# Performance work log

Measured on AMD Instinct MI355X. Metric: run time of the kernel, lower is better.

## Reference

```python
import jax, jax.numpy as jnp
import numpy as np

B, N, D = 2, 16384, 512
H = 256          # gated-attention hidden dim
C, K = 4, 8      # num classes, descriptions per class
EPS = 1e-12


def _l2norm(x):
    return x / jnp.clip(jnp.linalg.norm(x, axis=-1, keepdims=True), EPS)


def setup_inputs() -> dict:
    key = jax.random.key(0)
    ks = jax.random.split(key, 12)
    inp = {
        'x_s': jax.random.normal(ks[0], (B, N, D), jnp.float32),
        'coord_s': jax.random.uniform(ks[1], (B, N, 2), jnp.float32),
        'x_l': jax.random.normal(ks[2], (B, N, D), jnp.float32),
        'coord_l': jax.random.uniform(ks[3], (B, N, 2), jnp.float32),
        # visual_proj: Linear(D, D), stored as [in, out] (apply x @ W + b)
        'W_proj': jax.random.normal(ks[4], (D, D), jnp.float32) / np.sqrt(D),
        'b_proj': jnp.zeros((D,), jnp.float32),
        # frozen, L2-normalized text description features [C, K, D]
        'desc_feats': _l2norm(jax.random.normal(ks[5], (C, K, D), jnp.float32)),
        # GatedAttentionPooling params ([in, out] layout)
        'Wv': jax.random.normal(ks[6], (D, H), jnp.float32) / np.sqrt(D),
        'bv': jnp.zeros((H,), jnp.float32),
        'Wu': jax.random.normal(ks[7], (D, H), jnp.float32) / np.sqrt(D),
        'bu': jnp.zeros((H,), jnp.float32),
        'w_attn': jax.random.normal(ks[8], (H,), jnp.float32) / np.sqrt(H),
        'b_attn': jnp.zeros((), jnp.float32),
    }
    return inp


def _class_scores(xp, desc_feats):
    # xp: [B,N,D] normalized projected patches; desc_feats: [C,K,D]
    scale = desc_feats.shape[-1] ** (-0.5)
    sim = jnp.einsum('bnd,ckd->bnck', xp, desc_feats) * scale  # [B,N,C,K]
    attn = jax.nn.softmax(sim, axis=-1)
    # scores_c = <xp, attn @ desc_c> collapsed without materializing [B,N,C,D]
    return jnp.einsum('bnck,ckd,bnd->bnc', attn, desc_feats, xp)  # [B,N,C]


def _gated_pool(feats, Wv, bv, Wu, bu, w_attn, b_attn):
    # feats: [B,N,D]
    A_V = jnp.tanh(feats @ Wv + bv)                 # [B,N,H]
    A_U = jax.nn.sigmoid(feats @ Wu + bu)           # [B,N,H]
    A = (A_V * A_U) @ w_attn + b_attn               # [B,N]
    A = jax.nn.softmax(A, axis=1)
    return jnp.einsum('bn,bnd->bd', A, feats)       # [B,D]


def reference(x_s, coord_s, x_l, coord_l, W_proj, b_proj, desc_feats,
              Wv, bv, Wu, bu, w_attn, b_attn):
    # coords are unused by the compute path (kept for signature fidelity)
    x_s_proj = _l2norm(_l2norm(x_s) @ W_proj + b_proj)
    x_l_proj = _l2norm(_l2norm(x_l) @ W_proj + b_proj)

    class_scores_s = _class_scores(x_s_proj, desc_feats)  # [B,N,C]
    class_scores_l = _class_scores(x_l_proj, desc_feats)

    slide_s = _l2norm(_gated_pool(x_s_proj, Wv, bv, Wu, bu, w_attn, b_attn))
    slide_l = _l2norm(_gated_pool(x_l_proj, Wv, bv, Wu, bu, w_attn, b_attn))

    # text_features_low: per-class max over descriptions, L2-normalized
    text_feats = _l2norm(jnp.max(desc_feats, axis=1))      # [C,D]

    logits = slide_s @ text_feats.T + slide_l @ text_feats.T  # [B,C]
    Y_prob = jax.nn.softmax(logits, axis=1)
    Y_hat = jnp.argmax(Y_prob, axis=1)
    return Y_prob, Y_hat, class_scores_s, class_scores_l
```

## Files before the change

### kernel.cpp

```cpp
#include <hip/hip_runtime.h>
#include <math.h>

#define B_ 2
#define N_ 16384
#define D_ 512
#define C_ 4
#define K_ 8
#define ROWS (B_*N_)
#define ROWS2 (2*ROWS)
#define EPS_ 1e-12f

typedef unsigned short u16;
typedef unsigned int u32;
using short8  = __attribute__((ext_vector_type(8))) short;
using float4v = __attribute__((ext_vector_type(4))) float;

__device__ __forceinline__ u16 f2bf(float f) {
    union { float f; u32 u; } v; v.f = f;
    u32 r = v.u + 0x7fffu + ((v.u >> 16) & 1u);
    return (u16)(r >> 16);
}
__device__ __forceinline__ u32 pack2(float a, float b) {
    return (u32)f2bf(a) | ((u32)f2bf(b) << 16);
}
__device__ __forceinline__ float bf2f(u16 h) {
    union { u32 u; float f; } v; v.u = ((u32)h) << 16;
    return v.f;
}
__device__ __forceinline__ void load_lds16(const u16* g, u16* l) {
    __builtin_amdgcn_global_load_lds(
        (const __attribute__((address_space(1))) u32*)g,
        (__attribute__((address_space(3))) u32*)l, 16, 0, 0);
}
__device__ __forceinline__ void stage_rows8(const u16* gtile, u16* ldsTile, int g, int lane) {
    int rg = lane >> 3;
    int c  = (lane & 7) ^ rg;
    load_lds16(gtile + (size_t)(g * 8 + rg) * 512 + c * 8, ldsTile + g * 512);
}
#define AFRAG(lds, R, c) (*(const short8*)&(lds)[(R) * 64 + (((c) ^ ((R) & 7)) * 8)])

__global__ __launch_bounds__(256) void prep_weights_kernel(
    const float* __restrict__ Wp, const float* __restrict__ Wv, const float* __restrict__ Wu,
    const float* __restrict__ bv, const float* __restrict__ bu, const float* __restrict__ desc,
    u16* __restrict__ WpT, u16* __restrict__ WvuT, float* __restrict__ bvu,
    u16* __restrict__ descF)
{
    int idx = blockIdx.x * 256 + threadIdx.x;
    int n = idx >> 9, k = idx & 511;
    WpT[idx] = f2bf(Wp[k * 512 + n]);
    int tile = n >> 4, pair = tile >> 1, half = tile & 1, h = pair * 16 + (n & 15);
    WvuT[idx] = f2bf(half ? Wu[k * 256 + h] : Wv[k * 256 + h]);
    if (idx < 512) {
        int tl = idx >> 4, pr = tl >> 1, hf = tl & 1, hh = pr * 16 + (idx & 15);
        bvu[idx] = hf ? bu[hh] : bv[hh];
    }
    if (idx < 16384) {
        int j = idx & 7, l = (idx >> 3) & 63, g = (idx >> 9) & 1, kt = idx >> 10;
        descF[idx] = f2bf(desc[(size_t)(g * 16 + (l & 15)) * 512 + kt * 32 + (l >> 4) * 8 + j]);
    }
}

__global__ __launch_bounds__(256) void rownorm_cast_kernel(
    const float* __restrict__ x_s, const float* __restrict__ x_l, u16* __restrict__ xn)
{
    int wave = threadIdx.x >> 6, lane = threadIdx.x & 63;
    size_t row = (size_t)blockIdx.x * 4 + wave;
    const float* xr = (row < (size_t)ROWS) ? (x_s + row * D_)
                                           : (x_l + (row - ROWS) * D_);
    float4 a = *(const float4*)&xr[lane * 8];
    float4 b = *(const float4*)&xr[lane * 8 + 4];
    float s = a.x*a.x + a.y*a.y + a.z*a.z + a.w*a.w
            + b.x*b.x + b.y*b.y + b.z*b.z + b.w*b.w;
#pragma unroll
    for (int off = 32; off; off >>= 1) s += __shfl_xor(s, off, 64);
    float inv = 1.0f / fmaxf(sqrtf(s), EPS_);
    uint4 o;
    o.x = pack2(a.x * inv, a.y * inv);
    o.y = pack2(a.z * inv, a.w * inv);
    o.z = pack2(b.x * inv, b.y * inv);
    o.w = pack2(b.z * inv, b.w * inv);
    *(uint4*)&xn[row * D_ + lane * 8] = o;
}

__global__ __launch_bounds__(512, 2) void gemm_bias_kernel(
    const u16* __restrict__ A, const u16* __restrict__ Bt,
    const float* __restrict__ bias, u16* __restrict__ C)
{
    __shared__ u16 ldsA[128 * 64];
    __shared__ u16 ldsB[512 * 64];
    int t = threadIdx.x, wave = t >> 6, lane = t & 63;
    int lr = lane & 15, lq = lane >> 4;
    int wm = wave >> 2, wn = wave & 3;
    int M0 = blockIdx.x * 128;

    float4v acc[4][8];
#pragma unroll
    for (int i = 0; i < 4; ++i)
#pragma unroll
        for (int j = 0; j < 8; ++j)
#pragma unroll
            for (int r = 0; r < 4; ++r) acc[i][j][r] = 0.f;

    for (int k0 = 0; k0 < 512; k0 += 64) {
        const u16* Ab = A  + (size_t)M0 * 512 + k0;
        const u16* Bb = Bt + k0;
        stage_rows8(Ab, ldsA, wave * 2 + 0, lane);
        stage_rows8(Ab, ldsA, wave * 2 + 1, lane);
#pragma unroll
        for (int s = 0; s < 8; ++s) stage_rows8(Bb, ldsB, wave * 8 + s, lane);
        __syncthreads();
#pragma unroll
        for (int kt = 0; kt < 2; ++kt) {
            short8 af[4], bfr[8];
#pragma unroll
            for (int i = 0; i < 4; ++i)
                af[i] = AFRAG(ldsA, wm * 64 + i * 16 + lr, kt * 4 + lq);
#pragma unroll
            for (int j = 0; j < 8; ++j)
                bfr[j] = AFRAG(ldsB, wn * 128 + j * 16 + lr, kt * 4 + lq);
#pragma unroll
            for (int i = 0; i < 4; ++i)
#pragma unroll
                for (int j = 0; j < 8; ++j)
                    acc[i][j] = __builtin_amdgcn_mfma_f32_16x16x32_bf16(bfr[j], af[i], acc[i][j], 0, 0, 0);
        }
        __syncthreads();
    }

    int colbase = wn * 128;
    float4 b4[8];
#pragma unroll
    for (int j = 0; j < 8; ++j)
        b4[j] = *(const float4*)&bias[colbase + j * 16 + lq * 4];
#pragma unroll
    for (int i = 0; i < 4; ++i) {
        int m = M0 + wm * 64 + i * 16 + lr;
        u16* crow = C + (size_t)m * 512;
#pragma unroll
        for (int j = 0; j < 8; ++j) {
            int nb = colbase + j * 16 + lq * 4;
            uint2 o;
            o.x = pack2(acc[i][j][0] + b4[j].x, acc[i][j][1] + b4[j].y);
            o.y = pack2(acc[i][j][2] + b4[j].z, acc[i][j][3] + b4[j].w);
            *(uint2*)&crow[nb] = o;
        }
    }
}

__global__ __launch_bounds__(512, 2) void gatecls_kernel(
    const u16* __restrict__ A, const u16* __restrict__ Bt,
    const u16* __restrict__ descF,
    const float* __restrict__ bvu, const float* __restrict__ w_attn,
    float* __restrict__ invn, float* __restrict__ Araw,
    float* __restrict__ out10)
{
    __shared__ u16 ldsA[128 * 64];
    __shared__ u16 ldsB[512 * 64];
    int t = threadIdx.x, wave = t >> 6, lane = t & 63;
    int lr = lane & 15, lq = lane >> 4;
    int wm = wave >> 2, wn = wave & 3;
    int M0 = blockIdx.x * 128;

    float4v acc[4][8];
    float4v accS[2], accG;
#pragma unroll
    for (int i = 0; i < 4; ++i)
#pragma unroll
        for (int j = 0; j < 8; ++j)
#pragma unroll
            for (int r = 0; r < 4; ++r) acc[i][j][r] = 0.f;
#pragma unroll
    for (int r = 0; r < 4; ++r) { accS[0][r] = 0.f; accS[1][r] = 0.f; accG[r] = 0.f; }

    for (int k0 = 0; k0 < 512; k0 += 64) {
        const u16* Ab = A  + (size_t)M0 * 512 + k0;
        const u16* Bb = Bt + k0;
        stage_rows8(Ab, ldsA, wave * 2 + 0, lane);
        stage_rows8(Ab, ldsA, wave * 2 + 1, lane);
#pragma unroll
        for (int s = 0; s < 8; ++s) stage_rows8(Bb, ldsB, wave * 8 + s, lane);
        __syncthreads();
#pragma unroll
        for (int kt = 0; kt < 2; ++kt) {
            int ktg = (k0 >> 5) + kt;
            short8 d0 = *(const short8*)&descF[(ktg * 2 + 0) * 512 + lane * 8];
            short8 d1 = *(const short8*)&descF[(ktg * 2 + 1) * 512 + lane * 8];
            short8 afc = AFRAG(ldsA, wave * 16 + lr, kt * 4 + lq);
            accS[0] = __builtin_amdgcn_mfma_f32_16x16x32_bf16(afc, d0, accS[0], 0, 0, 0);
            accS[1] = __builtin_amdgcn_mfma_f32_16x16x32_bf16(afc, d1, accS[1], 0, 0, 0);
            accG    = __builtin_amdgcn_mfma_f32_16x16x32_bf16(afc, afc, accG, 0, 0, 0);
            short8 af[4], bfr[8];
#pragma unroll
            for (int i = 0; i < 4; ++i)
                af[i] = AFRAG(ldsA, wm * 64 + i * 16 + lr, kt * 4 + lq);
#pragma unroll
            for (int j = 0; j < 8; ++j)
                bfr[j] = AFRAG(ldsB, wn * 128 + j * 16 + lr, kt * 4 + lq);
#pragma unroll
            for (int i = 0; i < 4; ++i)
#pragma unroll
                for (int j = 0; j < 8; ++j)
                    acc[i][j] = __builtin_amdgcn_mfma_f32_16x16x32_bf16(bfr[j], af[i], acc[i][j], 0, 0, 0);
        }
        __syncthreads();
    }

    float* sInvF = (float*)ldsA;
    float* redA  = ((float*)ldsA) + 128;

#pragma unroll
    for (int r = 0; r < 4; ++r) {
        if (lr == lq * 4 + r) {
            float iv = 1.0f / fmaxf(sqrtf(accG[r]), EPS_);
            sInvF[wave * 16 + lq * 4 + r] = iv;
            invn[M0 + wave * 16 + lq * 4 + r] = iv;
        }
    }
    __syncthreads();

    {
        const float scale = 0.04419417382415922f;
        int side = (M0 >= ROWS) ? 1 : 0;
        float* cls = out10 + (size_t)side * ((size_t)ROWS * 4);
        int rbase = M0 - side * ROWS + wave * 16;
#pragma unroll
        for (int r = 0; r < 4; ++r) {
            int rloc = rbase + lq * 4 + r;
            float iv = sInvF[wave * 16 + lq * 4 + r];
            float sv0 = accS[0][r] * iv, sv1 = accS[1][r] * iv;
#pragma unroll
            for (int g = 0; g < 2; ++g) {
                float s = g ? sv1 : sv0;
                float ts = s * scale;
                float mx = ts;
                mx = fmaxf(mx, __shfl_xor(mx, 1, 64));
                mx = fmaxf(mx, __shfl_xor(mx, 2, 64));
                mx = fmaxf(mx, __shfl_xor(mx, 4, 64));
                float e = expf(ts - mx);
                float num = e * s, den = e;
                num += __shfl_xor(num, 1, 64); den += __shfl_xor(den, 1, 64);
                num += __shfl_xor(num, 2, 64); den += __shfl_xor(den, 2, 64);
                num += __shfl_xor(num, 4, 64); den += __shfl_xor(den, 4, 64);
                if ((lr & 7) == 0) {
                    int c = g * 2 + ((lr >> 3) & 1);
                    cls[(size_t)rloc * 4 + c] = num / den;
                }
            }
        }
    }

    int colbase = wn * 128;
    int hbase = colbase >> 1;
    float4 bv4[4], bu4[4], w4[4];
#pragma unroll
    for (int p = 0; p < 4; ++p) {
        int nv = colbase + p * 32 + lq * 4;
        bv4[p] = *(const float4*)&bvu[nv];
        bu4[p] = *(const float4*)&bvu[nv + 16];
        w4[p]  = *(const float4*)&w_attn[hbase + p * 16 + lq * 4];
    }
#pragma unroll
    for (int i = 0; i < 4; ++i) {
        int rloc = wm * 64 + i * 16 + lr;
        float iv = sInvF[rloc];
        float part = 0.f;
#pragma unroll
        for (int p = 0; p < 4; ++p) {
#pragma unroll
            for (int r = 0; r < 4; ++r) {
                float v = acc[i][2 * p][r] * iv + (&bv4[p].x)[r];
                float u = acc[i][2 * p + 1][r] * iv + (&bu4[p].x)[r];
                part += tanhf(v) * (&w4[p].x)[r] * (1.0f / (1.0f + expf(-u)));
            }
        }
        part += __shfl_xor(part, 16, 64);
        part += __shfl_xor(part, 32, 64);
        if (lq == 0) redA[wn * 128 + rloc] = part;
    }
    __syncthreads();
    if (t < 128) Araw[M0 + t] = redA[t] + redA[128 + t] + redA[256 + t] + redA[384 + t];
}

__global__ __launch_bounds__(256) void areduce_kernel(
    const float* __restrict__ Araw, float* __restrict__ part)
{
    __shared__ float red[256];
    int t = threadIdx.x, g = blockIdx.y;
    size_t i0 = (size_t)g * N_ + blockIdx.x * 512 + t * 2;
    float2 v = *(const float2*)&Araw[i0];
    red[t] = fmaxf(v.x, v.y); __syncthreads();
    for (int s = 128; s; s >>= 1) { if (t < s) red[t] = fmaxf(red[t], red[t + s]); __syncthreads(); }
    float m = red[0]; __syncthreads();
    red[t] = __expf(v.x - m) + __expf(v.y - m); __syncthreads();
    for (int s = 128; s; s >>= 1) { if (t < s) red[t] += red[t + s]; __syncthreads(); }
    if (t == 0) {
        int pi = g * 32 + blockIdx.x;
        part[pi * 2] = m;
        part[pi * 2 + 1] = red[0];
    }
}

__global__ __launch_bounds__(128) void acombine_kernel(
    const float* __restrict__ part, float* __restrict__ mg)
{
    int t = threadIdx.x;
    int g = t >> 5, j = t & 31;
    float m = part[(g * 32 + j) * 2];
    float s = part[(g * 32 + j) * 2 + 1];
    float mm = m;
#pragma unroll
    for (int off = 1; off < 32; off <<= 1) mm = fmaxf(mm, __shfl_xor(mm, off, 64));
    float sc = s * __expf(m - mm);
#pragma unroll
    for (int off = 1; off < 32; off <<= 1) sc += __shfl_xor(sc, off, 64);
    if (j == 0) {
        mg[g * 2] = mm;
        mg[g * 2 + 1] = 1.0f / sc;
    }
}

__global__ __launch_bounds__(256) void pool_kernel(
    const float* __restrict__ Araw, const float* __restrict__ invn,
    const float* __restrict__ mg, const u16* __restrict__ xpraw,
    float* __restrict__ slideAll)
{
    __shared__ float lds[4][512];
    int t = threadIdx.x, wave = t >> 6, lane = t & 63;
    int g = blockIdx.y;
    float m = mg[g * 2], is = mg[g * 2 + 1];
    size_t row0 = (size_t)g * N_ + (size_t)blockIdx.x * 256 + wave;
    float a[8] = {};
    for (int r = 0; r < 64; ++r) {
        size_t row = row0 + r * 4;
        float av = __expf(Araw[row] - m) * is * invn[row];
        uint4 pk = *(const uint4*)&xpraw[row * D_ + lane * 8];
        a[0] += av * bf2f((u16)pk.x); a[1] += av * bf2f((u16)(pk.x >> 16));
        a[2] += av * bf2f((u16)pk.y); a[3] += av * bf2f((u16)(pk.y >> 16));
        a[4] += av * bf2f((u16)pk.z); a[5] += av * bf2f((u16)(pk.z >> 16));
        a[6] += av * bf2f((u16)pk.w); a[7] += av * bf2f((u16)(pk.w >> 16));
    }
#pragma unroll
    for (int i = 0; i < 8; ++i) lds[wave][lane * 8 + i] = a[i];
    __syncthreads();
#pragma unroll
    for (int q = 0; q < 2; ++q) {
        int c = t * 2 + q;
        float s = lds[0][c] + lds[1][c] + lds[2][c] + lds[3][c];
        atomicAdd(&slideAll[(size_t)g * 512 + c], s);
    }
}

__global__ __launch_bounds__(512) void finalize_kernel(
    const float* __restrict__ slide_s, const float* __restrict__ slide_l,
    const float* __restrict__ desc, float* __restrict__ out)
{
    __shared__ float txt[4][512];
    __shared__ float ssn[2][512];
    __shared__ float sln[2][512];
    __shared__ float red[512];
    __shared__ float lg[8];
    int t = threadIdx.x;

    auto reduceSum = [&](float v) -> float {
        red[t] = v; __syncthreads();
        for (int s = 256; s; s >>= 1) { if (t < s) red[t] += red[t + s]; __syncthreads(); }
        float r = red[0]; __syncthreads();
        return r;
    };

    for (int c = 0; c < 4; ++c) {
        float m = -1e30f;
        for (int k = 0; k < 8; ++k) m = fmaxf(m, desc[((size_t)c * 8 + k) * 512 + t]);
        float ss = reduceSum(m * m);
        txt[c][t] = m / fmaxf(sqrtf(ss), EPS_);
    }
    for (int b = 0; b < 2; ++b) {
        float v = slide_s[b * 512 + t];
        float ss = reduceSum(v * v);
        ssn[b][t] = v / fmaxf(sqrtf(ss), EPS_);
        v = slide_l[b * 512 + t];
        ss = reduceSum(v * v);
        sln[b][t] = v / fmaxf(sqrtf(ss), EPS_);
    }
    __syncthreads();
    for (int b = 0; b < 2; ++b)
        for (int c = 0; c < 4; ++c) {
            float v = ssn[b][t] * txt[c][t] + sln[b][t] * txt[c][t];
            float s = reduceSum(v);
            if (t == 0) lg[b * 4 + c] = s;
        }
    __syncthreads();
    if (t < 2) {
        int b = t;
        float m = -1e30f;
        for (int c = 0; c < 4; ++c) m = fmaxf(m, lg[b * 4 + c]);
        float e[4]; float den = 0.f;
        for (int c = 0; c < 4; ++c) { e[c] = expf(lg[b * 4 + c] - m); den += e[c]; }
        int am = 0; float bm = -1.f;
        for (int c = 0; c < 4; ++c) {
            float pcl = e[c] / den;
            out[b * 4 + c] = pcl;
            if (pcl > bm) { bm = pcl; am = c; }
        }
        out[8 + b] = (float)am;
    }
}

extern "C" void kernel_launch(void* const* d_in, const int* in_sizes, int n_in,
                              void* d_out, int out_size, void* d_ws, size_t ws_size,
                              hipStream_t stream) {
    const float* x_s    = (const float*)d_in[0];
    const float* x_l    = (const float*)d_in[2];
    const float* W_proj = (const float*)d_in[4];
    const float* b_proj = (const float*)d_in[5];
    const float* desc   = (const float*)d_in[6];
    const float* Wv     = (const float*)d_in[7];
    const float* bv     = (const float*)d_in[8];
    const float* Wu     = (const float*)d_in[9];
    const float* bu     = (const float*)d_in[10];
    const float* w_attn = (const float*)d_in[11];
    float* out = (float*)d_out;

    char* w = (char*)d_ws;
    u16* xn        = (u16*)w;
    u16* xpraw     = (u16*)(w + 67108864);
    u16* WpT       = (u16*)(w + 134217728);
    u16* WvuT      = (u16*)(w + 134742016);
    u16* descF     = (u16*)(w + 135266304);
    float* bvu     = (float*)(w + 135299072);
    float* invn    = (float*)(w + 135301120);
    float* Araw    = (float*)(w + 135563264);
    float* part    = (float*)(w + 135825408);
    float* mg      = (float*)(w + 135826432);
    float* slideAll= (float*)(w + 135827456);

    hipMemsetAsync(slideAll, 0, 8192, stream);
    prep_weights_kernel<<<1024, 256, 0, stream>>>(W_proj, Wv, Wu, bv, bu, desc,
                                                  WpT, WvuT, bvu, descF);

    rownorm_cast_kernel<<<ROWS2 / 4, 256, 0, stream>>>(x_s, x_l, xn);
    gemm_bias_kernel<<<512, 512, 0, stream>>>(xn, WpT, b_proj, xpraw);
    gatecls_kernel<<<512, 512, 0, stream>>>(xpraw, WvuT, descF, bvu, w_attn,
                                            invn, Araw, out + 10);
    areduce_kernel<<<dim3(32, 4), 256, 0, stream>>>(Araw, part);
    acombine_kernel<<<1, 128, 0, stream>>>(part, mg);
    pool_kernel<<<dim3(64, 4), 256, 0, stream>>>(Araw, invn, mg, xpraw, slideAll);
    finalize_kernel<<<1, 512, 0, stream>>>(slideAll, slideAll + 1024, desc, out);
}
```

Before: 334.9 us.

## Split GEMMs into 128x128 N-tiles and move row norm into projection epilogue

Both GEMM kernels change from 128x512 tiles with 512 threads (512 blocks) to 128x128 tiles with 256 threads over a 4x512 grid. This raises block count and lowers the per-block LDS footprint, which should improve occupancy and load balance. The row sum-of-squares is now computed in the projection epilogue and accumulated with atomics, replacing the MFMA self-dot in gatecls; gate partials go to four per-N-tile buffers that areduce sums. The gate activations use fast __expf-based tanh and sigmoid. In exchange, A tiles are re-read four times per GEMM, and the change adds atomics and a larger memset.

```diff
diff --git a/kernel.cpp b/kernel.cpp
--- a/kernel.cpp
+++ b/kernel.cpp
@@ -27,6 +27,9 @@
     union { u32 u; float f; } v; v.u = ((u32)h) << 16;
     return v.f;
 }
+__device__ __forceinline__ float fsigmoid(float x) { return 1.0f / (1.0f + __expf(-x)); }
+__device__ __forceinline__ float ftanh(float x)    { return 1.0f - 2.0f / (__expf(2.0f * x) + 1.0f); }
+
 __device__ __forceinline__ void load_lds16(const u16* g, u16* l) {
     __builtin_amdgcn_global_load_lds(
         (const __attribute__((address_space(1))) u32*)g,
@@ -82,195 +85,200 @@
     *(uint4*)&xn[row * D_ + lane * 8] = o;
 }
 
-__global__ __launch_bounds__(512, 2) void gemm_bias_kernel(
+__global__ __launch_bounds__(256, 2) void gemm_bias_kernel(
     const u16* __restrict__ A, const u16* __restrict__ Bt,
-    const float* __restrict__ bias, u16* __restrict__ C)
+    const float* __restrict__ bias, u16* __restrict__ C, float* __restrict__ sumsq)
 {
     __shared__ u16 ldsA[128 * 64];
-    __shared__ u16 ldsB[512 * 64];
+    __shared__ u16 ldsB[128 * 64];
     int t = threadIdx.x, wave = t >> 6, lane = t & 63;
     int lr = lane & 15, lq = lane >> 4;
-    int wm = wave >> 2, wn = wave & 3;
-    int M0 = blockIdx.x * 128;
-
-    float4v acc[4][8];
+    int wm = wave >> 1, wn = wave & 1;
+    int M0 = blockIdx.y * 128, N0 = blockIdx.x * 128;
+
+    float4v acc[4][4];
 #pragma unroll
     for (int i = 0; i < 4; ++i)
 #pragma unroll
-        for (int j = 0; j < 8; ++j)
+        for (int j = 0; j < 4; ++j)
 #pragma unroll
             for (int r = 0; r < 4; ++r) acc[i][j][r] = 0.f;
 
     for (int k0 = 0; k0 < 512; k0 += 64) {
         const u16* Ab = A  + (size_t)M0 * 512 + k0;
-        const u16* Bb = Bt + k0;
-        stage_rows8(Ab, ldsA, wave * 2 + 0, lane);
-        stage_rows8(Ab, ldsA, wave * 2 + 1, lane);
-#pragma unroll
-        for (int s = 0; s < 8; ++s) stage_rows8(Bb, ldsB, wave * 8 + s, lane);
+        const u16* Bb = Bt + (size_t)N0 * 512 + k0;
+#pragma unroll
+        for (int s = 0; s < 4; ++s) stage_rows8(Ab, ldsA, wave * 4 + s, lane);
+#pragma unroll
+        for (int s = 0; s < 4; ++s) stage_rows8(Bb, ldsB, wave * 4 + s, lane);
         __syncthreads();
 #pragma unroll
         for (int kt = 0; kt < 2; ++kt) {
-            short8 af[4], bfr[8];
+            short8 af[4], bfr[4];
 #pragma unroll
             for (int i = 0; i < 4; ++i)
                 af[i] = AFRAG(ldsA, wm * 64 + i * 16 + lr, kt * 4 + lq);
 #pragma unroll
-            for (int j = 0; j < 8; ++j)
-                bfr[j] = AFRAG(ldsB, wn * 128 + j * 16 + lr, kt * 4 + lq);
+            for (int j = 0; j < 4; ++j)
+                bfr[j] = AFRAG(ldsB, wn * 64 + j * 16 + lr, kt * 4 + lq);
 #pragma unroll
             for (int i = 0; i < 4; ++i)
 #pragma unroll
-                for (int j = 0; j < 8; ++j)
+                for (int j = 0; j < 4; ++j)
                     acc[i][j] = __builtin_amdgcn_mfma_f32_16x16x32_bf16(bfr[j], af[i], acc[i][j], 0, 0, 0);
         }
         __syncthreads();
     }
 
-    int colbase = wn * 128;
-    float4 b4[8];
-#pragma unroll
-    for (int j = 0; j < 8; ++j)
-        b4[j] = *(const float4*)&bias[colbase + j * 16 + lq * 4];
+    float4 b4[4];
+#pragma unroll
+    for (int j = 0; j < 4; ++j)
+        b4[j] = *(const float4*)&bias[N0 + wn * 64 + j * 16 + lq * 4];
 #pragma unroll
     for (int i = 0; i < 4; ++i) {
         int m = M0 + wm * 64 + i * 16 + lr;
         u16* crow = C + (size_t)m * 512;
-#pragma unroll
-        for (int j = 0; j < 8; ++j) {
-            int nb = colbase + j * 16 + lq * 4;
+        float sq = 0.f;
+#pragma unroll
+        for (int j = 0; j < 4; ++j) {
+            int nb = N0 + wn * 64 + j * 16 + lq * 4;
+            float v0 = acc[i][j][0] + b4[j].x, v1 = acc[i][j][1] + b4[j].y;
+            float v2 = acc[i][j][2] + b4[j].z, v3 = acc[i][j][3] + b4[j].w;
+            u16 h0 = f2bf(v0), h1 = f2bf(v1), h2 = f2bf(v2), h3 = f2bf(v3);
             uint2 o;
-            o.x = pack2(acc[i][j][0] + b4[j].x, acc[i][j][1] + b4[j].y);
-            o.y = pack2(acc[i][j][2] + b4[j].z, acc[i][j][3] + b4[j].w);
+            o.x = (u32)h0 | ((u32)h1 << 16);
+            o.y = (u32)h2 | ((u32)h3 << 16);
             *(uint2*)&crow[nb] = o;
-        }
-    }
-}
-
-__global__ __launch_bounds__(512, 2) void gatecls_kernel(
+            float q0 = bf2f(h0), q1 = bf2f(h1), q2 = bf2f(h2), q3 = bf2f(h3);
+            sq += q0*q0 + q1*q1 + q2*q2 + q3*q3;
+        }
+        sq += __shfl_xor(sq, 16, 64);
+        sq += __shfl_xor(sq, 32, 64);
+        if (lq == 0) atomicAdd(&sumsq[m], sq);
+    }
+}
+
+__global__ __launch_bounds__(256, 2) void gatecls_kernel(
     const u16* __restrict__ A, const u16* __restrict__ Bt,
     const u16* __restrict__ descF,
     const float* __restrict__ bvu, const float* __restrict__ w_attn,
-    float* __restrict__ invn, float* __restrict__ Araw,
+    const float* __restrict__ sumsq, float* __restrict__ Araw4,
     float* __restrict__ out10)
 {
     __shared__ u16 ldsA[128 * 64];
-    __shared__ u16 ldsB[512 * 64];
+    __shared__ u16 ldsB[128 * 64];
     int t = threadIdx.x, wave = t >> 6, lane = t & 63;
     int lr = lane & 15, lq = lane >> 4;
-    int wm = wave >> 2, wn = wave & 3;
-    int M0 = blockIdx.x * 128;
-
-    float4v acc[4][8];
-    float4v accS[2], accG;
+    int wm = wave >> 1, wn = wave & 1;
+    int M0 = blockIdx.y * 128, N0 = blockIdx.x * 128;
+    const bool doCls = (blockIdx.x == 0);
+
+    float4v acc[4][4];
+    float4v accS[2][2];
 #pragma unroll
     for (int i = 0; i < 4; ++i)
 #pragma unroll
-        for (int j = 0; j < 8; ++j)
+        for (int j = 0; j < 4; ++j)
 #pragma unroll
             for (int r = 0; r < 4; ++r) acc[i][j][r] = 0.f;
 #pragma unroll
-    for (int r = 0; r < 4; ++r) { accS[0][r] = 0.f; accS[1][r] = 0.f; accG[r] = 0.f; }
+    for (int h = 0; h < 2; ++h)
+#pragma unroll
+        for (int r = 0; r < 4; ++r) { accS[h][0][r] = 0.f; accS[h][1][r] = 0.f; }
 
     for (int k0 = 0; k0 < 512; k0 += 64) {
         const u16* Ab = A  + (size_t)M0 * 512 + k0;
-        const u16* Bb = Bt + k0;
-        stage_rows8(Ab, ldsA, wave * 2 + 0, lane);
-        stage_rows8(Ab, ldsA, wave * 2 + 1, lane);
-#pragma unroll
-        for (int s = 0; s < 8; ++s) stage_rows8(Bb, ldsB, wave * 8 + s, lane);
+        const u16* Bb = Bt + (size_t)N0 * 512 + k0;
+#pragma unroll
+        for (int s = 0; s < 4; ++s) stage_rows8(Ab, ldsA, wave * 4 + s, lane);
+#pragma unroll
+        for (int s = 0; s < 4; ++s) stage_rows8(Bb, ldsB, wave * 4 + s, lane);
         __syncthreads();
 #pragma unroll
         for (int kt = 0; kt < 2; ++kt) {
-            int ktg = (k0 >> 5) + kt;
-            short8 d0 = *(const short8*)&descF[(ktg * 2 + 0) * 512 + lane * 8];
-            short8 d1 = *(const short8*)&descF[(ktg * 2 + 1) * 512 + lane * 8];
-            short8 afc = AFRAG(ldsA, wave * 16 + lr, kt * 4 + lq);
-            accS[0] = __builtin_amdgcn_mfma_f32_16x16x32_bf16(afc, d0, accS[0], 0, 0, 0);
-            accS[1] = __builtin_amdgcn_mfma_f32_16x16x32_bf16(afc, d1, accS[1], 0, 0, 0);
-            accG    = __builtin_amdgcn_mfma_f32_16x16x32_bf16(afc, afc, accG, 0, 0, 0);
-            short8 af[4], bfr[8];
+            if (doCls) {
+                int ktg = (k0 >> 5) + kt;
+                short8 d0 = *(const short8*)&descF[(ktg * 2 + 0) * 512 + lane * 8];
+                short8 d1 = *(const short8*)&descF[(ktg * 2 + 1) * 512 + lane * 8];
+#pragma unroll
+                for (int h = 0; h < 2; ++h) {
+                    short8 afc = AFRAG(ldsA, wave * 32 + h * 16 + lr, kt * 4 + lq);
+                    accS[h][0] = __builtin_amdgcn_mfma_f32_16x16x32_bf16(afc, d0, accS[h][0], 0, 0, 0);
+                    accS[h][1] = __builtin_amdgcn_mfma_f32_16x16x32_bf16(afc, d1, accS[h][1], 0, 0, 0);
+                }
+            }
+            short8 af[4], bfr[4];
 #pragma unroll
             for (int i = 0; i < 4; ++i)
                 af[i] = AFRAG(ldsA, wm * 64 + i * 16 + lr, kt * 4 + lq);
 #pragma unroll
-            for (int j = 0; j < 8; ++j)
-                bfr[j] = AFRAG(ldsB, wn * 128 + j * 16 + lr, kt * 4 + lq);
+            for (int j = 0; j < 4; ++j)
+                bfr[j] = AFRAG(ldsB, wn * 64 + j * 16 + lr, kt * 4 + lq);
 #pragma unroll
             for (int i = 0; i < 4; ++i)
 #pragma unroll
-                for (int j = 0; j < 8; ++j)
+                for (int j = 0; j < 4; ++j)
                     acc[i][j] = __builtin_amdgcn_mfma_f32_16x16x32_bf16(bfr[j], af[i], acc[i][j], 0, 0, 0);
         }
         __syncthreads();
     }
 
-    float* sInvF = (float*)ldsA;
-    float* redA  = ((float*)ldsA) + 128;
-
-#pragma unroll
-    for (int r = 0; r < 4; ++r) {
-        if (lr == lq * 4 + r) {
-            float iv = 1.0f / fmaxf(sqrtf(accG[r]), EPS_);
-            sInvF[wave * 16 + lq * 4 + r] = iv;
-            invn[M0 + wave * 16 + lq * 4 + r] = iv;
-        }
-    }
-    __syncthreads();
-
-    {
+    if (doCls) {
         const float scale = 0.04419417382415922f;
         int side = (M0 >= ROWS) ? 1 : 0;
         float* cls = out10 + (size_t)side * ((size_t)ROWS * 4);
-        int rbase = M0 - side * ROWS + wave * 16;
-#pragma unroll
-        for (int r = 0; r < 4; ++r) {
-            int rloc = rbase + lq * 4 + r;
-            float iv = sInvF[wave * 16 + lq * 4 + r];
-            float sv0 = accS[0][r] * iv, sv1 = accS[1][r] * iv;
-#pragma unroll
-            for (int g = 0; g < 2; ++g) {
-                float s = g ? sv1 : sv0;
-                float ts = s * scale;
-                float mx = ts;
-                mx = fmaxf(mx, __shfl_xor(mx, 1, 64));
-                mx = fmaxf(mx, __shfl_xor(mx, 2, 64));
-                mx = fmaxf(mx, __shfl_xor(mx, 4, 64));
-                float e = expf(ts - mx);
-                float num = e * s, den = e;
-                num += __shfl_xor(num, 1, 64); den += __shfl_xor(den, 1, 64);
-                num += __shfl_xor(num, 2, 64); den += __shfl_xor(den, 2, 64);
-                num += __shfl_xor(num, 4, 64); den += __shfl_xor(den, 4, 64);
-                if ((lr & 7) == 0) {
-                    int c = g * 2 + ((lr >> 3) & 1);
-                    cls[(size_t)rloc * 4 + c] = num / den;
+#pragma unroll
+        for (int h = 0; h < 2; ++h) {
+#pragma unroll
+            for (int r = 0; r < 4; ++r) {
+                int grow = M0 + wave * 32 + h * 16 + lq * 4 + r;
+                float iv = 1.0f / fmaxf(sqrtf(sumsq[grow]), EPS_);
+                float sv0 = accS[h][0][r] * iv, sv1 = accS[h][1][r] * iv;
+#pragma unroll
+                for (int g = 0; g < 2; ++g) {
+                    float s = g ? sv1 : sv0;
+                    float ts = s * scale;
+                    float mx = ts;
+                    mx = fmaxf(mx, __shfl_xor(mx, 1, 64));
+                    mx = fmaxf(mx, __shfl_xor(mx, 2, 64));
+                    mx = fmaxf(mx, __shfl_xor(mx, 4, 64));
+                    float e = __expf(ts - mx);
+                    float num = e * s, den = e;
+                    num += __shfl_xor(num, 1, 64); den += __shfl_xor(den, 1, 64);
+                    num += __shfl_xor(num, 2, 64); den += __shfl_xor(den, 2, 64);
+                    num += __shfl_xor(num, 4, 64); den += __shfl_xor(den, 4, 64);
+                    if ((lr & 7) == 0) {
+                        int c = g * 2 + ((lr >> 3) & 1);
+                        cls[(size_t)(grow - side * ROWS) * 4 + c] = num / den;
+                    }
                 }
             }
         }
     }
 
-    int colbase = wn * 128;
+    int colbase = N0 + wn * 64;
     int hbase = colbase >> 1;
-    float4 bv4[4], bu4[4], w4[4];
-#pragma unroll
-    for (int p = 0; p < 4; ++p) {
+    float4 bv4[2], bu4[2], w4[2];
+#pragma unroll
+    for (int p = 0; p < 2; ++p) {
         int nv = colbase + p * 32 + lq * 4;
         bv4[p] = *(const float4*)&bvu[nv];
         bu4[p] = *(const float4*)&bvu[nv + 16];
         w4[p]  = *(const float4*)&w_attn[hbase + p * 16 + lq * 4];
     }
+    float* redA = (float*)ldsA;
 #pragma unroll
     for (int i = 0; i < 4; ++i) {
         int rloc = wm * 64 + i * 16 + lr;
-        float iv = sInvF[rloc];
+        float iv = 1.0f / fmaxf(sqrtf(sumsq[M0 + rloc]), EPS_);
         float part = 0.f;
 #pragma unroll
-        for (int p = 0; p < 4; ++p) {
+        for (int p = 0; p < 2; ++p) {
 #pragma unroll
             for (int r = 0; r < 4; ++r) {
                 float v = acc[i][2 * p][r] * iv + (&bv4[p].x)[r];
                 float u = acc[i][2 * p + 1][r] * iv + (&bu4[p].x)[r];
-                part += tanhf(v) * (&w4[p].x)[r] * (1.0f / (1.0f + expf(-u)));
+                part += ftanh(v) * (&w4[p].x)[r] * fsigmoid(u);
             }
         }
         part += __shfl_xor(part, 16, 64);
@@ -278,20 +286,23 @@
         if (lq == 0) redA[wn * 128 + rloc] = part;
     }
     __syncthreads();
-    if (t < 128) Araw[M0 + t] = redA[t] + redA[128 + t] + redA[256 + t] + redA[384 + t];
+    if (t < 128)
+        Araw4[(size_t)blockIdx.x * ROWS2 + M0 + t] = redA[t] + redA[128 + t];
 }
 
 __global__ __launch_bounds__(256) void areduce_kernel(
-    const float* __restrict__ Araw, float* __restrict__ part)
+    float* __restrict__ Araw4, float* __restrict__ part)
 {
     __shared__ float red[256];
     int t = threadIdx.x, g = blockIdx.y;
     size_t i0 = (size_t)g * N_ + blockIdx.x * 512 + t * 2;
-    float2 v = *(const float2*)&Araw[i0];
-    red[t] = fmaxf(v.x, v.y); __syncthreads();
+    float v0 = Araw4[i0]     + Araw4[i0 + ROWS2]     + Araw4[i0 + 2*ROWS2]     + Araw4[i0 + 3*ROWS2];
+    float v1 = Araw4[i0 + 1] + Araw4[i0 + 1 + ROWS2] + Araw4[i0 + 1 + 2*ROWS2] + Araw4[i0 + 1 + 3*ROWS2];
+    *(float2*)&Araw4[i0] = make_float2(v0, v1);
+    red[t] = fmaxf(v0, v1); __syncthreads();
     for (int s = 128; s; s >>= 1) { if (t < s) red[t] = fmaxf(red[t], red[t + s]); __syncthreads(); }
     float m = red[0]; __syncthreads();
-    red[t] = __expf(v.x - m) + __expf(v.y - m); __syncthreads();
+    red[t] = __expf(v0 - m) + __expf(v1 - m); __syncthreads();
     for (int s = 128; s; s >>= 1) { if (t < s) red[t] += red[t + s]; __syncthreads(); }
     if (t == 0) {
         int pi = g * 32 + blockIdx.x;
@@ -320,7 +331,7 @@
 }
 
 __global__ __launch_bounds__(256) void pool_kernel(
-    const float* __restrict__ Araw, const float* __restrict__ invn,
+    const float* __restrict__ Araw, const float* __restrict__ sumsq,
     const float* __restrict__ mg, const u16* __restrict__ xpraw,
     float* __restrict__ slideAll)
 {
@@ -332,7 +343,8 @@
     float a[8] = {};
     for (int r = 0; r < 64; ++r) {
         size_t row = row0 + r * 4;
-        float av = __expf(Araw[row] - m) * is * invn[row];
+        float iv = 1.0f / fmaxf(sqrtf(sumsq[row]), EPS_);
+        float av = __expf(Araw[row] - m) * is * iv;
         uint4 pk = *(const uint4*)&xpraw[row * D_ + lane * 8];
         a[0] += av * bf2f((u16)pk.x); a[1] += av * bf2f((u16)(pk.x >> 16));
         a[2] += av * bf2f((u16)pk.y); a[3] += av * bf2f((u16)(pk.y >> 16));
@@ -428,22 +440,22 @@
     u16* WvuT      = (u16*)(w + 134742016);
     u16* descF     = (u16*)(w + 135266304);
     float* bvu     = (float*)(w + 135299072);
-    float* invn    = (float*)(w + 135301120);
-    float* Araw    = (float*)(w + 135563264);
-    float* part    = (float*)(w + 135825408);
-    float* mg      = (float*)(w + 135826432);
-    float* slideAll= (float*)(w + 135827456);
-
-    hipMemsetAsync(slideAll, 0, 8192, stream);
+    float* sumsq   = (float*)(w + 135301120);
+    float* slideAll= (float*)(w + 135563264);
+    float* Araw4   = (float*)(w + 135571456);
+    float* part    = (float*)(w + 136620032);
+    float* mg      = (float*)(w + 136621056);
+
+    hipMemsetAsync(sumsq, 0, 262144 + 8192, stream);
     prep_weights_kernel<<<1024, 256, 0, stream>>>(W_proj, Wv, Wu, bv, bu, desc,
                                                   WpT, WvuT, bvu, descF);
 
     rownorm_cast_kernel<<<ROWS2 / 4, 256, 0, stream>>>(x_s, x_l, xn);
-    gemm_bias_kernel<<<512, 512, 0, stream>>>(xn, WpT, b_proj, xpraw);
-    gatecls_kernel<<<512, 512, 0, stream>>>(xpraw, WvuT, descF, bvu, w_attn,
-                                            invn, Araw, out + 10);
-    areduce_kernel<<<dim3(32, 4), 256, 0, stream>>>(Araw, part);
+    gemm_bias_kernel<<<dim3(4, 512), 256, 0, stream>>>(xn, WpT, b_proj, xpraw, sumsq);
+    gatecls_kernel<<<dim3(4, 512), 256, 0, stream>>>(xpraw, WvuT, descF, bvu, w_attn,
+                                                     sumsq, Araw4, out + 10);
+    areduce_kernel<<<dim3(32, 4), 256, 0, stream>>>(Araw4, part);
     acombine_kernel<<<1, 128, 0, stream>>>(part, mg);
-    pool_kernel<<<dim3(64, 4), 256, 0, stream>>>(Araw, invn, mg, xpraw, slideAll);
+    pool_kernel<<<dim3(64, 4), 256, 0, stream>>>(Araw4, sumsq, mg, xpraw, slideAll);
     finalize_kernel<<<1, 512, 0, stream>>>(slideAll, slideAll + 1024, desc, out);
 }
```

Measured after the change: 352.1 us. 5.1% more time.

## Fuse projection GEMM and gate/class GEMM via LDS-resident tile, prepacked weight fragments

Applied to the files above, without the earlier changes.

Merges the projection GEMM and the gated-attention/class-score GEMM into one kernel. The bf16 projected 128x512 tile stays in LDS and feeds the second GEMM directly, so it is not re-read from global memory. Weights are prepacked into MFMA fragment order and read straight from global/L2 instead of being staged through LDS. It also swaps tanhf, expf and the sigmoid for fast __expf-based versions. The fused kernel uses about 144KB of LDS, which may lower occupancy to one block per CU, and the fast math functions lose some precision.

```diff
diff --git a/kernel.cpp b/kernel.cpp
--- a/kernel.cpp
+++ b/kernel.cpp
@@ -27,6 +27,9 @@
     union { u32 u; float f; } v; v.u = ((u32)h) << 16;
     return v.f;
 }
+__device__ __forceinline__ float fsigmoid(float x) { return 1.0f / (1.0f + __expf(-x)); }
+__device__ __forceinline__ float ftanh(float x)    { return 1.0f - 2.0f / (__expf(2.0f * x) + 1.0f); }
+
 __device__ __forceinline__ void load_lds16(const u16* g, u16* l) {
     __builtin_amdgcn_global_load_lds(
         (const __attribute__((address_space(1))) u32*)g,
@@ -38,25 +41,28 @@
     load_lds16(gtile + (size_t)(g * 8 + rg) * 512 + c * 8, ldsTile + g * 512);
 }
 #define AFRAG(lds, R, c) (*(const short8*)&(lds)[(R) * 64 + (((c) ^ ((R) & 7)) * 8)])
+#define BFRAG(Bf, nf, ks, lane) (*(const short8*)&(Bf)[((size_t)((nf) * 16 + (ks)) << 9) + ((lane) << 3)])
 
 __global__ __launch_bounds__(256) void prep_weights_kernel(
     const float* __restrict__ Wp, const float* __restrict__ Wv, const float* __restrict__ Wu,
     const float* __restrict__ bv, const float* __restrict__ bu, const float* __restrict__ desc,
-    u16* __restrict__ WpT, u16* __restrict__ WvuT, float* __restrict__ bvu,
+    u16* __restrict__ WpF, u16* __restrict__ WvuF, float* __restrict__ bvu,
     u16* __restrict__ descF)
 {
     int idx = blockIdx.x * 256 + threadIdx.x;
-    int n = idx >> 9, k = idx & 511;
-    WpT[idx] = f2bf(Wp[k * 512 + n]);
-    int tile = n >> 4, pair = tile >> 1, half = tile & 1, h = pair * 16 + (n & 15);
-    WvuT[idx] = f2bf(half ? Wu[k * 256 + h] : Wv[k * 256 + h]);
+    int e = idx & 7, l = (idx >> 3) & 63, ks = (idx >> 9) & 15, nf = idx >> 13;
+    int k = ks * 32 + ((l >> 4) << 3) + e;
+    int n = (nf << 4) + (l & 15);
+    WpF[idx] = f2bf(Wp[(size_t)k * 512 + n]);
+    int half = nf & 1, h = (nf >> 1) * 16 + (l & 15);
+    WvuF[idx] = f2bf(half ? Wu[(size_t)k * 256 + h] : Wv[(size_t)k * 256 + h]);
     if (idx < 512) {
         int tl = idx >> 4, pr = tl >> 1, hf = tl & 1, hh = pr * 16 + (idx & 15);
         bvu[idx] = hf ? bu[hh] : bv[hh];
     }
     if (idx < 16384) {
-        int j = idx & 7, l = (idx >> 3) & 63, g = (idx >> 9) & 1, kt = idx >> 10;
-        descF[idx] = f2bf(desc[(size_t)(g * 16 + (l & 15)) * 512 + kt * 32 + (l >> 4) * 8 + j]);
+        int j = idx & 7, dl = (idx >> 3) & 63, g = (idx >> 9) & 1, kt = idx >> 10;
+        descF[idx] = f2bf(desc[(size_t)(g * 16 + (dl & 15)) * 512 + kt * 32 + (dl >> 4) * 8 + j]);
     }
 }
 
@@ -82,132 +88,126 @@
     *(uint4*)&xn[row * D_ + lane * 8] = o;
 }
 
-__global__ __launch_bounds__(512, 2) void gemm_bias_kernel(
-    const u16* __restrict__ A, const u16* __restrict__ Bt,
-    const float* __restrict__ bias, u16* __restrict__ C)
-{
-    __shared__ u16 ldsA[128 * 64];
-    __shared__ u16 ldsB[512 * 64];
+__global__ __launch_bounds__(512, 2) void fused_kernel(
+    const u16* __restrict__ A,
+    const u16* __restrict__ BpF,
+    const u16* __restrict__ BvuF,
+    const u16* __restrict__ descF,
+    const float* __restrict__ bias,
+    const float* __restrict__ bvu, const float* __restrict__ w_attn,
+    u16* __restrict__ Cp,
+    float* __restrict__ invn, float* __restrict__ Araw,
+    float* __restrict__ out10)
+{
+    __shared__ u16 ldsStage[8192];
+    __shared__ u16 tile[65536];
     int t = threadIdx.x, wave = t >> 6, lane = t & 63;
     int lr = lane & 15, lq = lane >> 4;
     int wm = wave >> 2, wn = wave & 3;
     int M0 = blockIdx.x * 128;
-
-    float4v acc[4][8];
+    const u16* Arow = A + (size_t)M0 * 512;
+
+    float4v acc1[4][8];
 #pragma unroll
     for (int i = 0; i < 4; ++i)
 #pragma unroll
         for (int j = 0; j < 8; ++j)
 #pragma unroll
-            for (int r = 0; r < 4; ++r) acc[i][j][r] = 0.f;
-
-    for (int k0 = 0; k0 < 512; k0 += 64) {
-        const u16* Ab = A  + (size_t)M0 * 512 + k0;
-        const u16* Bb = Bt + k0;
-        stage_rows8(Ab, ldsA, wave * 2 + 0, lane);
-        stage_rows8(Ab, ldsA, wave * 2 + 1, lane);
-#pragma unroll
-        for (int s = 0; s < 8; ++s) stage_rows8(Bb, ldsB, wave * 8 + s, lane);
+            for (int r = 0; r < 4; ++r) acc1[i][j][r] = 0.f;
+
+#pragma unroll 1
+    for (int tt = 0; tt < 8; ++tt) {
+#pragma unroll
+        for (int s = 0; s < 2; ++s)
+            stage_rows8(Arow + tt * 64, ldsStage, wave * 2 + s, lane);
         __syncthreads();
 #pragma unroll
         for (int kt = 0; kt < 2; ++kt) {
+            int ks = tt * 2 + kt;
             short8 af[4], bfr[8];
 #pragma unroll
             for (int i = 0; i < 4; ++i)
-                af[i] = AFRAG(ldsA, wm * 64 + i * 16 + lr, kt * 4 + lq);
+                af[i] = AFRAG(ldsStage, wm * 64 + i * 16 + lr, kt * 4 + lq);
 #pragma unroll
             for (int j = 0; j < 8; ++j)
-                bfr[j] = AFRAG(ldsB, wn * 128 + j * 16 + lr, kt * 4 + lq);
+                bfr[j] = BFRAG(BpF, wn * 8 + j, ks, lane);
 #pragma unroll
             for (int i = 0; i < 4; ++i)
 #pragma unroll
                 for (int j = 0; j < 8; ++j)
-                    acc[i][j] = __builtin_amdgcn_mfma_f32_16x16x32_bf16(bfr[j], af[i], acc[i][j], 0, 0, 0);
+                    acc1[i][j] = __builtin_amdgcn_mfma_f32_16x16x32_bf16(bfr[j], af[i], acc1[i][j], 0, 0, 0);
         }
         __syncthreads();
     }
 
-    int colbase = wn * 128;
-    float4 b4[8];
-#pragma unroll
-    for (int j = 0; j < 8; ++j)
-        b4[j] = *(const float4*)&bias[colbase + j * 16 + lq * 4];
-#pragma unroll
-    for (int i = 0; i < 4; ++i) {
-        int m = M0 + wm * 64 + i * 16 + lr;
-        u16* crow = C + (size_t)m * 512;
-#pragma unroll
-        for (int j = 0; j < 8; ++j) {
-            int nb = colbase + j * 16 + lq * 4;
-            uint2 o;
-            o.x = pack2(acc[i][j][0] + b4[j].x, acc[i][j][1] + b4[j].y);
-            o.y = pack2(acc[i][j][2] + b4[j].z, acc[i][j][3] + b4[j].w);
-            *(uint2*)&crow[nb] = o;
-        }
-    }
-}
-
-__global__ __launch_bounds__(512, 2) void gatecls_kernel(
-    const u16* __restrict__ A, const u16* __restrict__ Bt,
-    const u16* __restrict__ descF,
-    const float* __restrict__ bvu, const float* __restrict__ w_attn,
-    float* __restrict__ invn, float* __restrict__ Araw,
-    float* __restrict__ out10)
-{
-    __shared__ u16 ldsA[128 * 64];
-    __shared__ u16 ldsB[512 * 64];
-    int t = threadIdx.x, wave = t >> 6, lane = t & 63;
-    int lr = lane & 15, lq = lane >> 4;
-    int wm = wave >> 2, wn = wave & 3;
-    int M0 = blockIdx.x * 128;
-
-    float4v acc[4][8];
+    {
+        float4 b4[8];
+#pragma unroll
+        for (int j = 0; j < 8; ++j)
+            b4[j] = *(const float4*)&bias[wn * 128 + j * 16 + lq * 4];
+#pragma unroll
+        for (int i = 0; i < 4; ++i) {
+            int row = wm * 64 + i * 16 + lr;
+            u16* crow = Cp + (size_t)(M0 + row) * 512;
+#pragma unroll
+            for (int j = 0; j < 8; ++j) {
+                int col = wn * 128 + j * 16 + lq * 4;
+                u16 h0 = f2bf(acc1[i][j][0] + b4[j].x);
+                u16 h1 = f2bf(acc1[i][j][1] + b4[j].y);
+                u16 h2 = f2bf(acc1[i][j][2] + b4[j].z);
+                u16 h3 = f2bf(acc1[i][j][3] + b4[j].w);
+                uint2 o;
+                o.x = (u32)h0 | ((u32)h1 << 16);
+                o.y = (u32)h2 | ((u32)h3 << 16);
+                *(uint2*)&crow[col] = o;
+                int kc = col >> 6, cc = col & 63;
+                int c8 = cc >> 3, off8 = cc & 7;
+                *(uint2*)&tile[kc * 8192 + row * 64 + ((c8 ^ (row & 7)) * 8) + off8] = o;
+            }
+        }
+    }
+    __syncthreads();
+
+    float4v acc2[4][8];
     float4v accS[2], accG;
 #pragma unroll
     for (int i = 0; i < 4; ++i)
 #pragma unroll
         for (int j = 0; j < 8; ++j)
 #pragma unroll
-            for (int r = 0; r < 4; ++r) acc[i][j][r] = 0.f;
+            for (int r = 0; r < 4; ++r) acc2[i][j][r] = 0.f;
 #pragma unroll
     for (int r = 0; r < 4; ++r) { accS[0][r] = 0.f; accS[1][r] = 0.f; accG[r] = 0.f; }
 
-    for (int k0 = 0; k0 < 512; k0 += 64) {
-        const u16* Ab = A  + (size_t)M0 * 512 + k0;
-        const u16* Bb = Bt + k0;
-        stage_rows8(Ab, ldsA, wave * 2 + 0, lane);
-        stage_rows8(Ab, ldsA, wave * 2 + 1, lane);
-#pragma unroll
-        for (int s = 0; s < 8; ++s) stage_rows8(Bb, ldsB, wave * 8 + s, lane);
-        __syncthreads();
+#pragma unroll 1
+    for (int tt = 0; tt < 8; ++tt) {
+        const u16* tch = tile + tt * 8192;
 #pragma unroll
         for (int kt = 0; kt < 2; ++kt) {
-            int ktg = (k0 >> 5) + kt;
-            short8 d0 = *(const short8*)&descF[(ktg * 2 + 0) * 512 + lane * 8];
-            short8 d1 = *(const short8*)&descF[(ktg * 2 + 1) * 512 + lane * 8];
-            short8 afc = AFRAG(ldsA, wave * 16 + lr, kt * 4 + lq);
+            int ks = tt * 2 + kt;
+            short8 afc = AFRAG(tch, wave * 16 + lr, kt * 4 + lq);
+            short8 d0 = *(const short8*)&descF[((ks * 2 + 0) << 9) + (lane << 3)];
+            short8 d1 = *(const short8*)&descF[((ks * 2 + 1) << 9) + (lane << 3)];
             accS[0] = __builtin_amdgcn_mfma_f32_16x16x32_bf16(afc, d0, accS[0], 0, 0, 0);
             accS[1] = __builtin_amdgcn_mfma_f32_16x16x32_bf16(afc, d1, accS[1], 0, 0, 0);
             accG    = __builtin_amdgcn_mfma_f32_16x16x32_bf16(afc, afc, accG, 0, 0, 0);
             short8 af[4], bfr[8];
 #pragma unroll
             for (int i = 0; i < 4; ++i)
-                af[i] = AFRAG(ldsA, wm * 64 + i * 16 + lr, kt * 4 + lq);
+                af[i] = AFRAG(tch, wm * 64 + i * 16 + lr, kt * 4 + lq);
 #pragma unroll
             for (int j = 0; j < 8; ++j)
-                bfr[j] = AFRAG(ldsB, wn * 128 + j * 16 + lr, kt * 4 + lq);
+                bfr[j] = BFRAG(BvuF, wn * 8 + j, ks, lane);
 #pragma unroll
             for (int i = 0; i < 4; ++i)
 #pragma unroll
                 for (int j = 0; j < 8; ++j)
-                    acc[i][j] = __builtin_amdgcn_mfma_f32_16x16x32_bf16(bfr[j], af[i], acc[i][j], 0, 0, 0);
-        }
-        __syncthreads();
-    }
-
-    float* sInvF = (float*)ldsA;
-    float* redA  = ((float*)ldsA) + 128;
-
+                    acc2[i][j] = __builtin_amdgcn_mfma_f32_16x16x32_bf16(bfr[j], af[i], acc2[i][j], 0, 0, 0);
+        }
+    }
+
+    float* sInvF = (float*)ldsStage;
+    float* redA  = ((float*)ldsStage) + 128;
 #pragma unroll
     for (int r = 0; r < 4; ++r) {
         if (lr == lq * 4 + r) {
@@ -236,7 +236,7 @@
                 mx = fmaxf(mx, __shfl_xor(mx, 1, 64));
                 mx = fmaxf(mx, __shfl_xor(mx, 2, 64));
                 mx = fmaxf(mx, __shfl_xor(mx, 4, 64));
-                float e = expf(ts - mx);
+                float e = __expf(ts - mx);
                 float num = e * s, den = e;
                 num += __shfl_xor(num, 1, 64); den += __shfl_xor(den, 1, 64);
                 num += __shfl_xor(num, 2, 64); den += __shfl_xor(den, 2, 64);
@@ -249,36 +249,39 @@
         }
     }
 
-    int colbase = wn * 128;
-    int hbase = colbase >> 1;
-    float4 bv4[4], bu4[4], w4[4];
-#pragma unroll
-    for (int p = 0; p < 4; ++p) {
-        int nv = colbase + p * 32 + lq * 4;
-        bv4[p] = *(const float4*)&bvu[nv];
-        bu4[p] = *(const float4*)&bvu[nv + 16];
-        w4[p]  = *(const float4*)&w_attn[hbase + p * 16 + lq * 4];
-    }
-#pragma unroll
-    for (int i = 0; i < 4; ++i) {
-        int rloc = wm * 64 + i * 16 + lr;
-        float iv = sInvF[rloc];
-        float part = 0.f;
+    {
+        int colbase = wn * 128;
+        int hbase = wn * 64;
+        float4 bv4[4], bu4[4], w4[4];
 #pragma unroll
         for (int p = 0; p < 4; ++p) {
-#pragma unroll
-            for (int r = 0; r < 4; ++r) {
-                float v = acc[i][2 * p][r] * iv + (&bv4[p].x)[r];
-                float u = acc[i][2 * p + 1][r] * iv + (&bu4[p].x)[r];
-                part += tanhf(v) * (&w4[p].x)[r] * (1.0f / (1.0f + expf(-u)));
+            int nv = colbase + p * 32 + lq * 4;
+            bv4[p] = *(const float4*)&bvu[nv];
+            bu4[p] = *(const float4*)&bvu[nv + 16];
+            w4[p]  = *(const float4*)&w_attn[hbase + p * 16 + lq * 4];
+        }
+#pragma unroll
+        for (int i = 0; i < 4; ++i) {
+            int rloc = wm * 64 + i * 16 + lr;
+            float iv = sInvF[rloc];
+            float part = 0.f;
+#pragma unroll
+            for (int p = 0; p < 4; ++p) {
+#pragma unroll
+                for (int r = 0; r < 4; ++r) {
+                    float v = acc2[i][2 * p][r] * iv + (&bv4[p].x)[r];
+                    float u = acc2[i][2 * p + 1][r] * iv + (&bu4[p].x)[r];
+                    part += ftanh(v) * (&w4[p].x)[r] * fsigmoid(u);
+                }
             }
-        }
-        part += __shfl_xor(part, 16, 64);
-        part += __shfl_xor(part, 32, 64);
-        if (lq == 0) redA[wn * 128 + rloc] = part;
-    }
-    __syncthreads();
-    if (t < 128) Araw[M0 + t] = redA[t] + redA[128 + t] + redA[256 + t] + redA[384 + t];
+            part += __shfl_xor(part, 16, 64);
+            part += __shfl_xor(part, 32, 64);
+            if (lq == 0) redA[wn * 128 + rloc] = part;
+        }
+    }
+    __syncthreads();
+    if (t < 128)
+        Araw[M0 + t] = redA[t] + redA[128 + t] + redA[256 + t] + redA[384 + t];
 }
 
 __global__ __launch_bounds__(256) void areduce_kernel(
@@ -424,8 +427,8 @@
     char* w = (char*)d_ws;
     u16* xn        = (u16*)w;
     u16* xpraw     = (u16*)(w + 67108864);
-    u16* WpT       = (u16*)(w + 134217728);
-    u16* WvuT      = (u16*)(w + 134742016);
+    u16* WpF       = (u16*)(w + 134217728);
+    u16* WvuF      = (u16*)(w + 134742016);
     u16* descF     = (u16*)(w + 135266304);
     float* bvu     = (float*)(w + 135299072);
     float* invn    = (float*)(w + 135301120);
@@ -436,12 +439,11 @@
 
     hipMemsetAsync(slideAll, 0, 8192, stream);
     prep_weights_kernel<<<1024, 256, 0, stream>>>(W_proj, Wv, Wu, bv, bu, desc,
-                                                  WpT, WvuT, bvu, descF);
+                                                  WpF, WvuF, bvu, descF);
 
     rownorm_cast_kernel<<<ROWS2 / 4, 256, 0, stream>>>(x_s, x_l, xn);
-    gemm_bias_kernel<<<512, 512, 0, stream>>>(xn, WpT, b_proj, xpraw);
-    gatecls_kernel<<<512, 512, 0, stream>>>(xpraw, WvuT, descF, bvu, w_attn,
-                                            invn, Araw, out + 10);
+    fused_kernel<<<512, 512, 0, stream>>>(xn, WpF, WvuF, descF, b_proj, bvu, w_attn,
+                                          xpraw, invn, Araw, out + 10);
     areduce_kernel<<<dim3(32, 4), 256, 0, stream>>>(Araw, part);
     acombine_kernel<<<1, 128, 0, stream>>>(part, mg);
     pool_kernel<<<dim3(64, 4), 256, 0, stream>>>(Araw, invn, mg, xpraw, slideAll);
```

Result: faster. 322.4 us (-3.7%).
